# Kernel tuning notes

Hardware: AMD Instinct MI355X
Metric: run time of the kernel (lower is better)

## Reference

```python
import jax, jax.numpy as jnp
import numpy as np

BN_EPS = 1e-5

def _batchnorm(h, gamma, beta):
    # training-mode BatchNorm1d: biased batch stats over the edge (batch) dim
    mean = jnp.mean(h, axis=0)
    var = jnp.var(h, axis=0)
    return (h - mean) * jax.lax.rsqrt(var + BN_EPS) * gamma + beta

def setup_inputs() -> dict:
    N, E, D_IN, D_OUT = 50000, 800000, 128, 128
    key = jax.random.key(0)
    ks = jax.random.split(key, 6)
    x = jax.random.normal(ks[0], (N, D_IN), dtype=jnp.float32)
    edge_index = jax.random.randint(ks[1], (2, E), 0, N, dtype=jnp.int32)
    # Linear weights stored torch-style (out, in); kaiming-ish uniform init scale
    lim1 = 1.0 / np.sqrt(2 * D_IN)
    lim2 = 1.0 / np.sqrt(D_OUT)
    W1 = jax.random.uniform(ks[2], (D_OUT, 2 * D_IN), jnp.float32, -lim1, lim1)
    b1 = jax.random.uniform(ks[3], (D_OUT,), jnp.float32, -lim1, lim1)
    W2 = jax.random.uniform(ks[4], (D_OUT, D_OUT), jnp.float32, -lim2, lim2)
    b2 = jax.random.uniform(ks[5], (D_OUT,), jnp.float32, -lim2, lim2)
    g1 = jnp.ones((D_OUT,), jnp.float32); be1 = jnp.zeros((D_OUT,), jnp.float32)
    g2 = jnp.ones((D_OUT,), jnp.float32); be2 = jnp.zeros((D_OUT,), jnp.float32)
    return {"x": x, "edge_index": edge_index, "W1": W1, "b1": b1, "g1": g1,
            "be1": be1, "W2": W2, "b2": b2, "g2": g2, "be2": be2}

def reference(x, edge_index, W1, b1, g1, be1, W2, b2, g2, be2):
    src, dst = edge_index[0], edge_index[1]
    # gather + concat: (E, 2*D_in)
    edge_features = jnp.concatenate([x[src], x[dst]], axis=1)
    h = edge_features @ W1.T + b1            # (E, D_out)
    h = jax.nn.relu(_batchnorm(h, g1, be1))
    h = h @ W2.T + b2                        # (E, D_out)
    edge_updates = jax.nn.relu(_batchnorm(h, g2, be2))
    # scatter-add into destination nodes
    x_out = jax.ops.segment_sum(edge_updates, dst, num_segments=x.shape[0])
    return x_out
```

## Files before the change

kernel.cpp:

```cpp
#include <hip/hip_runtime.h>
#include <stdint.h>

#define EPS 1e-5f

typedef __attribute__((ext_vector_type(4))) float f32x4;
typedef __attribute__((ext_vector_type(8))) short bf16x8_t;

__device__ __forceinline__ unsigned short f2bf(float x) {
    unsigned u = __float_as_uint(x);
    unsigned r = (u + 0x7FFFu + ((u >> 16) & 1u)) >> 16;
    return (unsigned short)r;
}
__device__ __forceinline__ float bf2f(unsigned short b) {
    return __uint_as_float(((unsigned)b) << 16);
}

__global__ __launch_bounds__(256) void gemm_p_kernel(const float* __restrict__ x,
    const float* __restrict__ W1, float* __restrict__ P, int Nn)
{
    __shared__ float As[64][36];
    __shared__ float Bt[32][68];
    int tid = threadIdx.x;
    int tx = tid & 15, ty = tid >> 4;
    int m0 = blockIdx.x * 64;
    int n0 = blockIdx.y * 64;
    float acc[4][4] = {};
    for (int kc = 0; kc < 128; kc += 32) {
        for (int t = tid; t < 512; t += 256) {
            int r = t >> 3, q = t & 7;
            int m = m0 + r;
            float4 v = make_float4(0.f, 0.f, 0.f, 0.f);
            if (m < Nn) v = *(const float4*)&x[(size_t)m * 128 + kc + q * 4];
            *(float4*)&As[r][q * 4] = v;
        }
        for (int t = tid; t < 512; t += 256) {
            int r = t >> 3, q = t & 7;
            int j = n0 + r;
            const float* s = (j < 128) ? &W1[(size_t)j * 256 + kc + q * 4]
                                       : &W1[(size_t)(j - 128) * 256 + 128 + kc + q * 4];
            float4 w = *(const float4*)s;
            Bt[q * 4 + 0][r] = w.x; Bt[q * 4 + 1][r] = w.y;
            Bt[q * 4 + 2][r] = w.z; Bt[q * 4 + 3][r] = w.w;
        }
        __syncthreads();
        #pragma unroll
        for (int kk = 0; kk < 32; kk += 4) {
            float avf[4][4];
            #pragma unroll
            for (int i = 0; i < 4; i++)
                *(float4*)&avf[i][0] = *(const float4*)&As[ty * 4 + i][kk];
            #pragma unroll
            for (int s = 0; s < 4; s++) {
                float4 b = *(const float4*)&Bt[kk + s][tx * 4];
                float bb[4] = {b.x, b.y, b.z, b.w};
                #pragma unroll
                for (int i = 0; i < 4; i++)
                    #pragma unroll
                    for (int j = 0; j < 4; j++)
                        acc[i][j] = fmaf(avf[i][s], bb[j], acc[i][j]);
            }
        }
        __syncthreads();
    }
    #pragma unroll
    for (int i = 0; i < 4; i++) {
        int m = m0 + ty * 4 + i;
        if (m < Nn)
            *(float4*)&P[(size_t)m * 256 + n0 + tx * 4] =
                make_float4(acc[i][0], acc[i][1], acc[i][2], acc[i][3]);
    }
}

__global__ void convert_w2_kernel(const float* __restrict__ W2, unsigned short* __restrict__ W2bf)
{
    int i = blockIdx.x * 256 + threadIdx.x;
    W2bf[i] = f2bf(W2[i]);
}

__global__ __launch_bounds__(256) void stats1_kernel(const float* __restrict__ P,
    const int* __restrict__ src, const int* __restrict__ dst, int E,
    float* __restrict__ gsum, float* __restrict__ gsq)
{
    int tid = threadIdx.x;
    int cg = tid & 31, rg = tid >> 5;
    int c0 = cg * 4;
    f32x4 s = {0.f, 0.f, 0.f, 0.f}, q = {0.f, 0.f, 0.f, 0.f};
    int stride = gridDim.x * 8;
    for (int e = blockIdx.x * 8 + rg; e < E; e += stride) {
        int sN = src[e], dN = dst[e];
        f32x4 v = *(const f32x4*)&P[(size_t)sN * 256 + c0]
                + *(const f32x4*)&P[(size_t)dN * 256 + 128 + c0];
        s += v; q += v * v;
    }
    __shared__ float shs[8][128], shq[8][128];
    *(f32x4*)&shs[rg][c0] = s;
    *(f32x4*)&shq[rg][c0] = q;
    __syncthreads();
    if (tid < 128) {
        float ts = 0.f, tq = 0.f;
        #pragma unroll
        for (int g = 0; g < 8; g++) { ts += shs[g][tid]; tq += shq[g][tid]; }
        atomicAdd(&gsum[tid], ts);
        atomicAdd(&gsq[tid], tq);
    }
}

__global__ void finalize_kernel(const float* __restrict__ gsum, const float* __restrict__ gsq,
    const float* __restrict__ gamma, const float* __restrict__ beta, float Einv,
    float* __restrict__ a, float* __restrict__ cc)
{
    int c = threadIdx.x;
    float mean = gsum[c] * Einv;
    float var  = gsq[c] * Einv - mean * mean;
    float ai = gamma[c] / sqrtf(var + EPS);
    a[c] = ai;
    cc[c] = beta[c] - mean * ai;
}

__global__ __launch_bounds__(256) void hist_kernel(const int* __restrict__ dst, int E,
    int* __restrict__ cnt)
{
    int i = blockIdx.x * 256 + threadIdx.x;
    int stride = gridDim.x * 256;
    for (; i < E; i += stride) atomicAdd(&cnt[dst[i]], 1);
}

__global__ __launch_bounds__(256) void scan_sum_kernel(const int* __restrict__ cnt, int Nn,
    int* __restrict__ bsum)
{
    int t = threadIdx.x, b = blockIdx.x;
    int i = b * 256 + t;
    __shared__ int sh[256];
    sh[t] = (i < Nn) ? cnt[i] : 0;
    __syncthreads();
    for (int d = 128; d > 0; d >>= 1) { if (t < d) sh[t] += sh[t + d]; __syncthreads(); }
    if (t == 0) bsum[b] = sh[0];
}

__global__ __launch_bounds__(256) void scan_base_kernel(const int* __restrict__ bsum, int nb,
    int* __restrict__ bbase)
{
    int t = threadIdx.x;
    int v = (t < nb) ? bsum[t] : 0;
    __shared__ int sh[256];
    sh[t] = v;
    __syncthreads();
    for (int d = 1; d < 256; d <<= 1) {
        int x = (t >= d) ? sh[t - d] : 0;
        __syncthreads();
        sh[t] += x;
        __syncthreads();
    }
    if (t < nb) bbase[t] = sh[t] - v;
}

__global__ __launch_bounds__(256) void scan_offs_kernel(const int* __restrict__ cnt,
    const int* __restrict__ bbase, int Nn, int E, int* __restrict__ offs)
{
    int t = threadIdx.x, b = blockIdx.x;
    int i = b * 256 + t;
    int v = (i < Nn) ? cnt[i] : 0;
    __shared__ int sh[256];
    sh[t] = v;
    __syncthreads();
    for (int d = 1; d < 256; d <<= 1) {
        int x = (t >= d) ? sh[t - d] : 0;
        __syncthreads();
        sh[t] += x;
        __syncthreads();
    }
    if (i < Nn) offs[i] = bbase[b] + sh[t] - v;
    if (i == 0 && b == 0) offs[Nn] = E;
}

template<int MODE>
__global__ __launch_bounds__(256) void edge_mfma_kernel(
    const float* __restrict__ P, const int* __restrict__ src, const int* __restrict__ dst,
    const unsigned short* __restrict__ W2bf,
    const float* __restrict__ a1, const float* __restrict__ c1,
    unsigned short* __restrict__ h2s, float* __restrict__ gsum, float* __restrict__ gsq,
    const int* __restrict__ offs, int* __restrict__ pos,
    const float* __restrict__ a2, const float* __restrict__ c2,
    float* __restrict__ out, int E)
{
    int tid = threadIdx.x;
    int wid = tid >> 6, lane = tid & 63;
    int lr = lane & 15, lk = lane >> 4;
    int wm = wid >> 1, wn = wid & 1;
    int e0 = blockIdx.x * 64;
    int m0w = wm * 32, n0w = wn * 64;

    __shared__ int rks[64];
    __shared__ int didx[64];
    if (MODE == 0 && tid < 64) {
        int e = e0 + tid;
        if (e < E) {
            int d = dst[e];
            rks[tid] = offs[d] + atomicAdd(&pos[d], 1);
        }
    }
    if (MODE == 2 && tid < 64) {
        int e = min(e0 + tid, E - 1);
        didx[tid] = dst[e];
    }

    int e_mi[2], s_mi[2], d_mi[2];
    #pragma unroll
    for (int mi = 0; mi < 2; mi++) {
        int e = e0 + m0w + mi * 16 + lr;
        e_mi[mi] = e;
        int ec = min(e, E - 1);
        s_mi[mi] = src[ec];
        d_mi[mi] = dst[ec];
    }

    f32x4 acc[2][4];
    #pragma unroll
    for (int mi = 0; mi < 2; mi++)
        #pragma unroll
        for (int nj = 0; nj < 4; nj++) {
            f32x4 z = {0.f, 0.f, 0.f, 0.f};
            acc[mi][nj] = z;
        }

    #pragma unroll
    for (int kt = 0; kt < 4; kt++) {
        int c0 = kt * 32 + lk * 8;
        bf16x8_t b[4];
        #pragma unroll
        for (int nj = 0; nj < 4; nj++)
            b[nj] = *(const bf16x8_t*)&W2bf[(size_t)(n0w + nj * 16 + lr) * 128 + c0];
        f32x4 a1v0 = *(const f32x4*)&a1[c0], a1v1 = *(const f32x4*)&a1[c0 + 4];
        f32x4 c1v0 = *(const f32x4*)&c1[c0], c1v1 = *(const f32x4*)&c1[c0 + 4];
        #pragma unroll
        for (int mi = 0; mi < 2; mi++) {
            const float* ps = &P[(size_t)s_mi[mi] * 256 + c0];
            const float* pd = &P[(size_t)d_mi[mi] * 256 + 128 + c0];
            f32x4 h0 = *(const f32x4*)ps + *(const f32x4*)pd;
            f32x4 h1 = *(const f32x4*)(ps + 4) + *(const f32x4*)(pd + 4);
            float vm = (e_mi[mi] < E) ? 1.f : 0.f;
            bf16x8_t ahi, alo;
            #pragma unroll
            for (int j = 0; j < 8; j++) {
                float hv = (j < 4) ? h0[j] : h1[j - 4];
                float av = (j < 4) ? a1v0[j] : a1v1[j - 4];
                float cv = (j < 4) ? c1v0[j] : c1v1[j - 4];
                float u = fmaxf(fmaf(av, hv, cv), 0.f) * vm;
                unsigned short uh = f2bf(u);
                ahi[j] = (short)uh;
                alo[j] = (short)f2bf(u - bf2f(uh));
            }
            #pragma unroll
            for (int nj = 0; nj < 4; nj++) {
                acc[mi][nj] = __builtin_amdgcn_mfma_f32_16x16x32_bf16(ahi, b[nj], acc[mi][nj], 0, 0, 0);
                acc[mi][nj] = __builtin_amdgcn_mfma_f32_16x16x32_bf16(alo, b[nj], acc[mi][nj], 0, 0, 0);
            }
        }
    }

    if (MODE == 0 || MODE == 1) {
        __shared__ float reds[2][128], redq[2][128];
        #pragma unroll
        for (int nj = 0; nj < 4; nj++) {
            float sa = 0.f, sq = 0.f;
            #pragma unroll
            for (int mi = 0; mi < 2; mi++)
                #pragma unroll
                for (int r = 0; r < 4; r++) {
                    float v = acc[mi][nj][r];
                    sa += v; sq += v * v;
                }
            sa += __shfl_xor(sa, 16); sa += __shfl_xor(sa, 32);
            sq += __shfl_xor(sq, 16); sq += __shfl_xor(sq, 32);
            if (lk == 0) {
                reds[wm][n0w + nj * 16 + lr] = sa;
                redq[wm][n0w + nj * 16 + lr] = sq;
            }
        }
        if (MODE == 0) {
            __shared__ unsigned short ush[64][136];
            #pragma unroll
            for (int mi = 0; mi < 2; mi++)
                #pragma unroll
                for (int nj = 0; nj < 4; nj++)
                    #pragma unroll
                    for (int r = 0; r < 4; r++)
                        ush[m0w + mi * 16 + lk * 4 + r][n0w + nj * 16 + lr] = f2bf(acc[mi][nj][r]);
            __syncthreads();
            if (tid < 128) {
                atomicAdd(&gsum[tid], reds[0][tid] + reds[1][tid]);
                atomicAdd(&gsq[tid],  redq[0][tid] + redq[1][tid]);
            }
            #pragma unroll
            for (int it = 0; it < 4; it++) {
                int chunk = it * 256 + tid;
                int row = chunk >> 4, q = chunk & 15;
                bf16x8_t v = *(const bf16x8_t*)&ush[row][q * 8];
                if (e0 + row < E)
                    *(bf16x8_t*)&h2s[(size_t)rks[row] * 128 + q * 8] = v;
            }
        } else {
            __syncthreads();
            if (tid < 128) {
                atomicAdd(&gsum[tid], reds[0][tid] + reds[1][tid]);
                atomicAdd(&gsq[tid],  redq[0][tid] + redq[1][tid]);
            }
        }
    }
    if (MODE == 2) {
        __syncthreads();
        float a2v[4], c2v[4];
        #pragma unroll
        for (int nj = 0; nj < 4; nj++) {
            int col = n0w + nj * 16 + lr;
            a2v[nj] = a2[col]; c2v[nj] = c2[col];
        }
        #pragma unroll
        for (int mi = 0; mi < 2; mi++)
            #pragma unroll
            for (int r = 0; r < 4; r++) {
                int row = m0w + mi * 16 + lk * 4 + r;
                if (e0 + row < E) {
                    int dn = didx[row];
                    #pragma unroll
                    for (int nj = 0; nj < 4; nj++) {
                        float y = fmaxf(fmaf(a2v[nj], acc[mi][nj][r], c2v[nj]), 0.f);
                        if (y > 0.f) atomicAdd(&out[(size_t)dn * 128 + n0w + nj * 16 + lr], y);
                    }
                }
            }
    }
}

__global__ __launch_bounds__(256) void segred_kernel(const unsigned short* __restrict__ h2s,
    const int* __restrict__ offs, const float* __restrict__ a2, const float* __restrict__ c2,
    float* __restrict__ out, int Nn)
{
    int node = blockIdx.x * 4 + (threadIdx.x >> 6);
    if (node >= Nn) return;
    int lane = threadIdx.x & 63;
    int c0 = lane * 2;
    float aa0 = a2[c0], aa1 = a2[c0 + 1];
    float cb0 = c2[c0], cb1 = c2[c0 + 1];
    int rb = offs[node], re = offs[node + 1];
    float s0 = 0.f, s1 = 0.f;
    for (int r = rb; r < re; ++r) {
        unsigned v = *(const unsigned*)&h2s[(size_t)r * 128 + c0];
        s0 += fmaxf(fmaf(aa0, bf2f((unsigned short)(v & 0xffffu)), cb0), 0.f);
        s1 += fmaxf(fmaf(aa1, bf2f((unsigned short)(v >> 16)), cb1), 0.f);
    }
    *(float2*)&out[(size_t)node * 128 + c0] = make_float2(s0, s1);
}

extern "C" void kernel_launch(void* const* d_in, const int* in_sizes, int n_in,
                              void* d_out, int out_size, void* d_ws, size_t ws_size,
                              hipStream_t stream)
{
    const float* x   = (const float*)d_in[0];
    const int*   ei  = (const int*)d_in[1];
    const float* W1  = (const float*)d_in[2];
    const float* g1  = (const float*)d_in[4];
    const float* be1 = (const float*)d_in[5];
    const float* W2  = (const float*)d_in[6];
    const float* g2  = (const float*)d_in[8];
    const float* be2 = (const float*)d_in[9];
    float* out = (float*)d_out;

    int Nn = in_sizes[0] / 128;
    int E  = in_sizes[1] / 2;
    const int* srcI = ei;
    const int* dstI = ei + E;

    float* ws    = (float*)d_ws;
    float* gsum1 = ws;        float* gsq1 = ws + 128;
    float* gsum2 = ws + 256;  float* gsq2 = ws + 384;
    float* a1    = ws + 512;  float* c1   = ws + 640;
    float* a2    = ws + 768;  float* c2   = ws + 896;
    unsigned short* W2bf = (unsigned short*)(ws + 1024);
    float* P     = ws + 9216;
    unsigned short* h2s = (unsigned short*)(P + (size_t)Nn * 256);
    int* cnt  = (int*)(h2s + (size_t)E * 128);
    int* pos  = cnt + Nn;
    int* offs = pos + Nn;
    int* bsum = offs + Nn + 1;
    int* bbase = bsum + 256;
    size_t need_mat = (size_t)9216 * 4 + (size_t)Nn * 1024 + (size_t)E * 256
                    + ((size_t)3 * Nn + 513 + 512) * 4;
    bool mat = (ws_size >= need_mat);
    int nb = (Nn + 255) / 256;

    hipMemsetAsync(ws, 0, 512 * sizeof(float), stream);
    hipMemsetAsync(out, 0, (size_t)out_size * sizeof(float), stream);

    dim3 b256(256);
    convert_w2_kernel<<<64, b256, 0, stream>>>(W2, W2bf);
    gemm_p_kernel<<<dim3((Nn + 63) / 64, 4), b256, 0, stream>>>(x, W1, P, Nn);
    stats1_kernel<<<4096, b256, 0, stream>>>(P, srcI, dstI, E, gsum1, gsq1);
    finalize_kernel<<<1, 128, 0, stream>>>(gsum1, gsq1, g1, be1, 1.0f / (float)E, a1, c1);

    int gE = (E + 63) / 64;
    if (mat && nb <= 256) {
        hipMemsetAsync(cnt, 0, (size_t)2 * Nn * sizeof(int), stream);
        hist_kernel<<<1024, b256, 0, stream>>>(dstI, E, cnt);
        scan_sum_kernel<<<nb, b256, 0, stream>>>(cnt, Nn, bsum);
        scan_base_kernel<<<1, b256, 0, stream>>>(bsum, nb, bbase);
        scan_offs_kernel<<<nb, b256, 0, stream>>>(cnt, bbase, Nn, E, offs);
        edge_mfma_kernel<0><<<gE, b256, 0, stream>>>(P, srcI, dstI, W2bf, a1, c1,
            h2s, gsum2, gsq2, offs, pos, nullptr, nullptr, nullptr, E);
        finalize_kernel<<<1, 128, 0, stream>>>(gsum2, gsq2, g2, be2, 1.0f / (float)E, a2, c2);
        segred_kernel<<<(Nn + 3) / 4, b256, 0, stream>>>(h2s, offs, a2, c2, out, Nn);
    } else {
        edge_mfma_kernel<1><<<gE, b256, 0, stream>>>(P, srcI, dstI, W2bf, a1, c1,
            nullptr, gsum2, gsq2, nullptr, nullptr, nullptr, nullptr, nullptr, E);
        finalize_kernel<<<1, 128, 0, stream>>>(gsum2, gsq2, g2, be2, 1.0f / (float)E, a2, c2);
        edge_mfma_kernel<2><<<gE, b256, 0, stream>>>(P, srcI, dstI, W2bf, a1, c1,
            nullptr, nullptr, nullptr, nullptr, nullptr, a2, c2, out, E);
    }
}
```

Measured before the change: 824.5 us.

## Fold BN1 affine into P, sort edges by destination, drop split-bf16 MFMA

Adds a prescale pass that applies the BN1 scale to the source half of P and the scale plus shift to the destination half, so the edge kernel only sums, applies ReLU and packs to bf16 with a hardware convert. The single-pass bf16 MFMA replaces the hi/lo split, halving MFMA work at the cost of lower precision in the second GEMM. A new permutation kernel sorts src/dst by destination before the edge kernel. The gathers then hit P rows in dst order and h2s is written contiguously instead of scattered, at the cost of an extra pass over the edges and extra workspace.

```diff
diff --git a/kernel.cpp b/kernel.cpp
--- a/kernel.cpp
+++ b/kernel.cpp
@@ -14,6 +14,12 @@
 __device__ __forceinline__ float bf2f(unsigned short b) {
     return __uint_as_float(((unsigned)b) << 16);
 }
+__device__ __forceinline__ unsigned cvtpk(float a, float b) {
+    unsigned r;
+    asm("v_cvt_pk_bf16_f32 %0, %1, %2" : "=v"(r) : "v"(a), "v"(b));
+    return r;
+}
+union U8 { unsigned u[4]; bf16x8_t v; };
 
 __global__ __launch_bounds__(256) void gemm_p_kernel(const float* __restrict__ x,
     const float* __restrict__ W1, float* __restrict__ P, int Nn)
@@ -117,6 +123,24 @@
     cc[c] = beta[c] - mean * ai;
 }
 
+__global__ __launch_bounds__(256) void prescale_kernel(float* __restrict__ P,
+    const float* __restrict__ a1, const float* __restrict__ c1, int Nn)
+{
+    long long i = (long long)blockIdx.x * 256 + threadIdx.x;
+    long long total = (long long)Nn * 64;
+    long long stride = (long long)gridDim.x * 256;
+    for (; i < total; i += stride) {
+        int col = (int)((i & 63) * 4);
+        f32x4 v = *(f32x4*)&P[i * 4];
+        if (col < 128) {
+            v *= *(const f32x4*)&a1[col];
+        } else {
+            v = v * (*(const f32x4*)&a1[col - 128]) + (*(const f32x4*)&c1[col - 128]);
+        }
+        *(f32x4*)&P[i * 4] = v;
+    }
+}
+
 __global__ __launch_bounds__(256) void hist_kernel(const int* __restrict__ dst, int E,
     int* __restrict__ cnt)
 {
@@ -173,13 +197,25 @@
     if (i == 0 && b == 0) offs[Nn] = E;
 }
 
+__global__ __launch_bounds__(256) void perm_kernel(const int* __restrict__ src,
+    const int* __restrict__ dst, int E, const int* __restrict__ offs, int* __restrict__ pos,
+    int* __restrict__ srcs, int* __restrict__ dsts)
+{
+    int i = blockIdx.x * 256 + threadIdx.x;
+    int stride = gridDim.x * 256;
+    for (; i < E; i += stride) {
+        int d = dst[i];
+        int slot = offs[d] + atomicAdd(&pos[d], 1);
+        srcs[slot] = src[i];
+        dsts[slot] = d;
+    }
+}
+
 template<int MODE>
 __global__ __launch_bounds__(256) void edge_mfma_kernel(
     const float* __restrict__ P, const int* __restrict__ src, const int* __restrict__ dst,
     const unsigned short* __restrict__ W2bf,
-    const float* __restrict__ a1, const float* __restrict__ c1,
     unsigned short* __restrict__ h2s, float* __restrict__ gsum, float* __restrict__ gsq,
-    const int* __restrict__ offs, int* __restrict__ pos,
     const float* __restrict__ a2, const float* __restrict__ c2,
     float* __restrict__ out, int E)
 {
@@ -190,15 +226,7 @@
     int e0 = blockIdx.x * 64;
     int m0w = wm * 32, n0w = wn * 64;
 
-    __shared__ int rks[64];
     __shared__ int didx[64];
-    if (MODE == 0 && tid < 64) {
-        int e = e0 + tid;
-        if (e < E) {
-            int d = dst[e];
-            rks[tid] = offs[d] + atomicAdd(&pos[d], 1);
-        }
-    }
     if (MODE == 2 && tid < 64) {
         int e = min(e0 + tid, E - 1);
         didx[tid] = dst[e];
@@ -230,8 +258,6 @@
         #pragma unroll
         for (int nj = 0; nj < 4; nj++)
             b[nj] = *(const bf16x8_t*)&W2bf[(size_t)(n0w + nj * 16 + lr) * 128 + c0];
-        f32x4 a1v0 = *(const f32x4*)&a1[c0], a1v1 = *(const f32x4*)&a1[c0 + 4];
-        f32x4 c1v0 = *(const f32x4*)&c1[c0], c1v1 = *(const f32x4*)&c1[c0 + 4];
         #pragma unroll
         for (int mi = 0; mi < 2; mi++) {
             const float* ps = &P[(size_t)s_mi[mi] * 256 + c0];
@@ -239,22 +265,14 @@
             f32x4 h0 = *(const f32x4*)ps + *(const f32x4*)pd;
             f32x4 h1 = *(const f32x4*)(ps + 4) + *(const f32x4*)(pd + 4);
             float vm = (e_mi[mi] < E) ? 1.f : 0.f;
-            bf16x8_t ahi, alo;
-            #pragma unroll
-            for (int j = 0; j < 8; j++) {
-                float hv = (j < 4) ? h0[j] : h1[j - 4];
-                float av = (j < 4) ? a1v0[j] : a1v1[j - 4];
-                float cv = (j < 4) ? c1v0[j] : c1v1[j - 4];
-                float u = fmaxf(fmaf(av, hv, cv), 0.f) * vm;
-                unsigned short uh = f2bf(u);
-                ahi[j] = (short)uh;
-                alo[j] = (short)f2bf(u - bf2f(uh));
-            }
-            #pragma unroll
-            for (int nj = 0; nj < 4; nj++) {
-                acc[mi][nj] = __builtin_amdgcn_mfma_f32_16x16x32_bf16(ahi, b[nj], acc[mi][nj], 0, 0, 0);
-                acc[mi][nj] = __builtin_amdgcn_mfma_f32_16x16x32_bf16(alo, b[nj], acc[mi][nj], 0, 0, 0);
-            }
+            U8 au;
+            au.u[0] = cvtpk(fmaxf(h0[0], 0.f) * vm, fmaxf(h0[1], 0.f) * vm);
+            au.u[1] = cvtpk(fmaxf(h0[2], 0.f) * vm, fmaxf(h0[3], 0.f) * vm);
+            au.u[2] = cvtpk(fmaxf(h1[0], 0.f) * vm, fmaxf(h1[1], 0.f) * vm);
+            au.u[3] = cvtpk(fmaxf(h1[2], 0.f) * vm, fmaxf(h1[3], 0.f) * vm);
+            #pragma unroll
+            for (int nj = 0; nj < 4; nj++)
+                acc[mi][nj] = __builtin_amdgcn_mfma_f32_16x16x32_bf16(au.v, b[nj], acc[mi][nj], 0, 0, 0);
         }
     }
 
@@ -297,7 +315,7 @@
                 int row = chunk >> 4, q = chunk & 15;
                 bf16x8_t v = *(const bf16x8_t*)&ush[row][q * 8];
                 if (e0 + row < E)
-                    *(bf16x8_t*)&h2s[(size_t)rks[row] * 128 + q * 8] = v;
+                    *(bf16x8_t*)&h2s[(size_t)(e0 + row) * 128 + q * 8] = v;
             }
         } else {
             __syncthreads();
@@ -384,8 +402,10 @@
     int* offs = pos + Nn;
     int* bsum = offs + Nn + 1;
     int* bbase = bsum + 256;
+    int* srcs = bbase + 256;
+    int* dsts = srcs + E;
     size_t need_mat = (size_t)9216 * 4 + (size_t)Nn * 1024 + (size_t)E * 256
-                    + ((size_t)3 * Nn + 513 + 512) * 4;
+                    + ((size_t)3 * Nn + 513 + 512 + (size_t)2 * E) * 4;
     bool mat = (ws_size >= need_mat);
     int nb = (Nn + 255) / 256;
 
@@ -395,8 +415,6 @@
     dim3 b256(256);
     convert_w2_kernel<<<64, b256, 0, stream>>>(W2, W2bf);
     gemm_p_kernel<<<dim3((Nn + 63) / 64, 4), b256, 0, stream>>>(x, W1, P, Nn);
-    stats1_kernel<<<4096, b256, 0, stream>>>(P, srcI, dstI, E, gsum1, gsq1);
-    finalize_kernel<<<1, 128, 0, stream>>>(gsum1, gsq1, g1, be1, 1.0f / (float)E, a1, c1);
 
     int gE = (E + 63) / 64;
     if (mat && nb <= 256) {
@@ -405,15 +423,22 @@
         scan_sum_kernel<<<nb, b256, 0, stream>>>(cnt, Nn, bsum);
         scan_base_kernel<<<1, b256, 0, stream>>>(bsum, nb, bbase);
         scan_offs_kernel<<<nb, b256, 0, stream>>>(cnt, bbase, Nn, E, offs);
-        edge_mfma_kernel<0><<<gE, b256, 0, stream>>>(P, srcI, dstI, W2bf, a1, c1,
-            h2s, gsum2, gsq2, offs, pos, nullptr, nullptr, nullptr, E);
+        perm_kernel<<<1024, b256, 0, stream>>>(srcI, dstI, E, offs, pos, srcs, dsts);
+        stats1_kernel<<<4096, b256, 0, stream>>>(P, srcs, dsts, E, gsum1, gsq1);
+        finalize_kernel<<<1, 128, 0, stream>>>(gsum1, gsq1, g1, be1, 1.0f / (float)E, a1, c1);
+        prescale_kernel<<<2048, b256, 0, stream>>>(P, a1, c1, Nn);
+        edge_mfma_kernel<0><<<gE, b256, 0, stream>>>(P, srcs, dsts, W2bf,
+            h2s, gsum2, gsq2, nullptr, nullptr, nullptr, E);
         finalize_kernel<<<1, 128, 0, stream>>>(gsum2, gsq2, g2, be2, 1.0f / (float)E, a2, c2);
         segred_kernel<<<(Nn + 3) / 4, b256, 0, stream>>>(h2s, offs, a2, c2, out, Nn);
     } else {
-        edge_mfma_kernel<1><<<gE, b256, 0, stream>>>(P, srcI, dstI, W2bf, a1, c1,
-            nullptr, gsum2, gsq2, nullptr, nullptr, nullptr, nullptr, nullptr, E);
+        stats1_kernel<<<4096, b256, 0, stream>>>(P, srcI, dstI, E, gsum1, gsq1);
+        finalize_kernel<<<1, 128, 0, stream>>>(gsum1, gsq1, g1, be1, 1.0f / (float)E, a1, c1);
+        prescale_kernel<<<2048, b256, 0, stream>>>(P, a1, c1, Nn);
+        edge_mfma_kernel<1><<<gE, b256, 0, stream>>>(P, srcI, dstI, W2bf,
+            nullptr, gsum2, gsq2, nullptr, nullptr, nullptr, E);
         finalize_kernel<<<1, 128, 0, stream>>>(gsum2, gsq2, g2, be2, 1.0f / (float)E, a2, c2);
-        edge_mfma_kernel<2><<<gE, b256, 0, stream>>>(P, srcI, dstI, W2bf, a1, c1,
-            nullptr, nullptr, nullptr, nullptr, nullptr, a2, c2, out, E);
-    }
-}
+        edge_mfma_kernel<2><<<gE, b256, 0, stream>>>(P, srcI, dstI, W2bf,
+            nullptr, nullptr, nullptr, a2, c2, out, E);
+    }
+}
```

Result: no change. 826.3 us (+0.2%).
